# Optimization experiments

Hardware: AMD Instinct MI355X
Metric: run time of the kernel (lower is better)

Reference implementation:

```python
import jax, jax.numpy as jnp
import numpy as np

B, T, HS = 2, 2048, 4096
H, HK, D = 32, 8, 128  # num_heads, num_kv_heads, head_dim; HS == H*D
N_REP = H // HK


def setup_inputs() -> dict:
    key = jax.random.key(0)
    k1, k2, k3 = jax.random.split(key, 3)
    x = jax.random.normal(k1, (B, T, HS), dtype=jnp.float32)
    # qkv Linear (no bias): out_features = HS + 2*HK*D
    W_qkv = jax.random.normal(k2, (HS + 2 * HK * D, HS), dtype=jnp.float32) * 0.02
    W_proj = jax.random.normal(k3, (HS, HS), dtype=jnp.float32) * 0.02
    # Realistic RoPE cache (rotate-half convention): [1, T, 1, D]
    pos = jnp.arange(T, dtype=jnp.float32)
    inv_freq = 1.0 / (10000.0 ** (jnp.arange(0, D, 2, dtype=jnp.float32) / D))
    ang = pos[:, None] * inv_freq[None, :]                      # [T, D/2]
    rope_cos = jnp.concatenate([jnp.cos(ang), jnp.cos(ang)], -1)[None, :, None, :]
    rope_sin = jnp.concatenate([jnp.sin(ang), jnp.sin(ang)], -1)[None, :, None, :]
    return {"x": x, "rope_cos": rope_cos, "rope_sin": rope_sin,
            "W_qkv": W_qkv, "W_proj": W_proj}


def _rotate_half(u):
    u1, u2 = jnp.split(u, 2, axis=-1)
    return jnp.concatenate([-u2, u1], axis=-1)


def _apply_rope(u, cos, sin):
    return u * cos + _rotate_half(u) * sin


def reference(x, rope_cos, rope_sin, W_qkv, W_proj):
    # fused QKV projection
    qkv = jnp.einsum('btc,oc->bto', x, W_qkv)
    q, k, v = jnp.split(qkv, [HS, HS + HK * D], axis=-1)
    q = q.reshape(B, T, H, D)
    k = k.reshape(B, T, HK, D)
    v = v.reshape(B, T, HK, D)
    # inline RoPE on q and k
    q = _apply_rope(q, rope_cos[:, :T], rope_sin[:, :T])
    k = _apply_rope(k, rope_cos[:, :T], rope_sin[:, :T])
    # GQA repeat_kv: [B,T,HK,D] -> [B,T,H,D]
    k = jnp.repeat(k, N_REP, axis=2)
    v = jnp.repeat(v, N_REP, axis=2)
    # causal attention (flash-equivalent math)
    scale = 1.0 / jnp.sqrt(jnp.asarray(D, dtype=q.dtype))
    scores = jnp.einsum('bqhd,bkhd->bhqk', q, k) * scale        # [B,H,T,T]
    causal = jnp.tril(jnp.ones((T, T), dtype=bool))
    scores = jnp.where(causal[None, None], scores, jnp.finfo(scores.dtype).min)
    p = jax.nn.softmax(scores, axis=-1)
    out = jnp.einsum('bhqk,bkhd->bqhd', p, v).reshape(B, T, HS)
    return jnp.einsum('btc,oc->bto', out, W_proj)
```

## Files before the change

kernel.cpp:

```cpp
#include <hip/hip_runtime.h>
#include <hip/hip_bf16.h>

typedef __attribute__((ext_vector_type(8))) short short8;
typedef __attribute__((ext_vector_type(4))) short short4v;
typedef __attribute__((ext_vector_type(4))) float floatx4;

__device__ __forceinline__ float b2f(ushort u) {
  unsigned x = ((unsigned)u) << 16;
  return __builtin_bit_cast(float, x);
}
__device__ __forceinline__ ushort f2b(float f) {
  unsigned x = __builtin_bit_cast(unsigned, f);
  x += 0x7fffu + ((x >> 16) & 1u);
  return (ushort)(x >> 16);
}

__device__ __forceinline__ void gload_lds16(const void* g, void* l) {
  __builtin_amdgcn_global_load_lds(
      (const __attribute__((address_space(1))) unsigned int*)g,
      (__attribute__((address_space(3))) unsigned int*)l, 16, 0, 0);
}

__global__ __launch_bounds__(256) void cvt_kernel(const float* __restrict__ in,
                                                  ushort* __restrict__ out, long n) {
  long i0 = ((long)blockIdx.x * 256 + threadIdx.x) * 4;
  long stride = (long)gridDim.x * 256 * 4;
  for (long i = i0; i < n; i += stride) {
    float4 v = *(const float4*)(in + i);
    ushort4 u;
    u.x = f2b(v.x); u.y = f2b(v.y); u.z = f2b(v.z); u.w = f2b(v.w);
    *(ushort4*)(out + i) = u;
  }
}

template <int BN, int OUTBF16>
__global__ __launch_bounds__(512, 2)
void gemm_pipe(const ushort* __restrict__ A, const ushort* __restrict__ B,
               float* __restrict__ Cf, ushort* __restrict__ Cb,
               int M, int N, int K) {
  constexpr int BNF = BN / 64;
  __shared__ __align__(16) ushort sA[2][256 * 64];
  __shared__ __align__(16) ushort sB[2][BN * 64];
  const int t = threadIdx.x;
  const int lane = t & 63;
  const int L = lane & 15, g = lane >> 4;
  const int w = t >> 6;
  const int wr = w >> 2, wc = w & 3;
  const int ntn = N / BN;
  const int nwg = gridDim.x;
  const int wg = blockIdx.x;
  const int swz = (wg & 7) * (nwg >> 3) + (wg >> 3);
  const int m0 = (swz / ntn) << 8;
  const int n0 = (swz % ntn) * BN;

  floatx4 acc[8][BNF];
#pragma unroll
  for (int i = 0; i < 8; i++)
#pragma unroll
    for (int j = 0; j < BNF; j++) acc[i][j] = (floatx4)(0.0f);

  const ushort* Ab = A + (size_t)m0 * K;
  const ushort* Bb = B + (size_t)n0 * K;

  auto stage_tile = [&](const ushort* Ag, const ushort* Bg, int buf) {
#pragma unroll
    for (int j = 0; j < 4; j++) {
      const int c = j * 512 + t;
      const int row = c >> 3, ch = c & 7;
      const int kc = ch ^ (row & 7);
      gload_lds16(Ag + (size_t)row * K + kc * 8, (char*)&sA[buf][0] + c * 16);
    }
#pragma unroll
    for (int j = 0; j < BNF; j++) {
      const int c = j * 512 + t;
      const int row = c >> 3, ch = c & 7;
      const int kc = ch ^ (row & 7);
      gload_lds16(Bg + (size_t)row * K + kc * 8, (char*)&sB[buf][0] + c * 16);
    }
  };
  auto rdA = [&](int buf, int mh, int kc16, short8* dst) {
#pragma unroll
    for (int i = 0; i < 4; i++) {
      const int row = wr * 128 + mh * 64 + i * 16 + L;
      const int ch = (kc16 * 4 + g) ^ (row & 7);
      dst[i] = *(const short8*)((const char*)&sA[buf][0] + row * 128 + ch * 16);
    }
  };
  auto rdB = [&](int buf, int kc16, short8* dst) {
#pragma unroll
    for (int i = 0; i < BNF; i++) {
      const int row = wc * (BN / 4) + i * 16 + L;
      const int ch = (kc16 * 4 + g) ^ (row & 7);
      dst[i] = *(const short8*)((const char*)&sB[buf][0] + row * 128 + ch * 16);
    }
  };

  short8 a0[4], a1[4], b0[BNF], b1[BNF];

  auto mfmaN = [&](short8* af, short8* bf, int accbase, int cnt) {
    __builtin_amdgcn_s_setprio(1);
    for (int i = 0; i < cnt; i++)
#pragma unroll
      for (int nf = 0; nf < BNF; nf++)
        acc[accbase + i][nf] =
            __builtin_amdgcn_mfma_f32_16x16x32_bf16(af[i], bf[nf], acc[accbase + i][nf], 0, 0, 0);
    __builtin_amdgcn_s_setprio(0);
  };

  const int NT = K >> 6;
  stage_tile(Ab, Bb, 0);
  __syncthreads();
  rdA(0, 0, 0, a0);
  rdB(0, 0, b0);

  for (int T = 0; T < NT; ++T) {
    const int p = T & 1, q = p ^ 1;
    const bool more = (T + 1 < NT);
    if (more) stage_tile(Ab + (T + 1) * 64, Bb + (T + 1) * 64, q);
    rdA(p, 1, 0, a1);
    mfmaN(a0, b0, 0, 4);
    rdA(p, 0, 1, a0);
    rdB(p, 1, b1);
    mfmaN(a1, b0, 4, 4);
    rdA(p, 1, 1, a1);
    mfmaN(a0, b1, 0, 4);
    mfmaN(a1, b1, 4, 2);
    __syncthreads();
    if (more) {
      rdA(q, 0, 0, a0);
      rdB(q, 0, b0);
    }
    mfmaN(a1 + 2, b1, 6, 2);
  }

#pragma unroll
  for (int mf = 0; mf < 8; mf++)
#pragma unroll
    for (int nf = 0; nf < BNF; nf++)
#pragma unroll
      for (int r = 0; r < 4; r++) {
        const int row = m0 + wr * 128 + mf * 16 + g * 4 + r;
        const int col = n0 + wc * (BN / 4) + nf * 16 + L;
        if (OUTBF16)
          Cb[(size_t)row * N + col] = f2b(acc[mf][nf][r]);
        else
          Cf[(size_t)row * N + col] = acc[mf][nf][r];
      }
}

__global__ __launch_bounds__(256)
void rope_kernel(const ushort* __restrict__ qkv, const float* __restrict__ cosp,
                 const float* __restrict__ sinp, ushort* __restrict__ Qo,
                 ushort* __restrict__ Ko) {
  const int row = blockIdx.x;
  const int b = row >> 11, tt = row & 2047;
  const int i = threadIdx.x;
  const ushort* qr = qkv + (size_t)row * 6144;

  const int jb = (i & 7) * 8;
  float cs[8], sn[8];
  *(float4*)&cs[0] = *(const float4*)(cosp + tt * 128 + jb);
  *(float4*)&cs[4] = *(const float4*)(cosp + tt * 128 + jb + 4);
  *(float4*)&sn[0] = *(const float4*)(sinp + tt * 128 + jb);
  *(float4*)&sn[4] = *(const float4*)(sinp + tt * 128 + jb + 4);

  {
    const int hh = i >> 3;
    short8 lo = *(const short8*)(qr + hh * 128 + jb);
    short8 hi = *(const short8*)(qr + hh * 128 + 64 + jb);
    short8 olo, ohi;
#pragma unroll
    for (int e = 0; e < 8; e++) {
      float fl = b2f((ushort)lo[e]), fh = b2f((ushort)hi[e]);
      olo[e] = (short)f2b(fl * cs[e] - fh * sn[e]);
      ohi[e] = (short)f2b(fh * cs[e] + fl * sn[e]);
    }
    ushort* dst = Qo + ((size_t)(b * 32 + hh) * 2048 + tt) * 128 + jb;
    *(short8*)dst = olo;
    *(short8*)(dst + 64) = ohi;
  }
  if (i < 64) {
    const int hkk = i >> 3;
    short8 lo = *(const short8*)(qr + 4096 + hkk * 128 + jb);
    short8 hi = *(const short8*)(qr + 4096 + hkk * 128 + 64 + jb);
    short8 olo, ohi;
#pragma unroll
    for (int e = 0; e < 8; e++) {
      float fl = b2f((ushort)lo[e]), fh = b2f((ushort)hi[e]);
      olo[e] = (short)f2b(fl * cs[e] - fh * sn[e]);
      ohi[e] = (short)f2b(fh * cs[e] + fl * sn[e]);
    }
    ushort* dst = Ko + ((size_t)(b * 8 + hkk) * 2048 + tt) * 128 + jb;
    *(short8*)dst = olo;
    *(short8*)(dst + 64) = ohi;
  }
}

__global__ __launch_bounds__(256)
void vtrans_kernel(const ushort* __restrict__ qkv, ushort* __restrict__ Vt) {
  const int bx = blockIdx.x;
  const int t0 = (bx & 31) * 64;
  const int hk = (bx >> 5) & 7;
  const int b = bx >> 8;
  const int i = threadIdx.x;
  const int tq = i & 15;
  const int dn = i >> 4;
  const ushort* src = qkv + ((size_t)(b * 2048 + t0 + tq * 4)) * 6144 + 5120 + hk * 128 + dn * 8;
  short8 v0 = *(const short8*)(src);
  short8 v1 = *(const short8*)(src + 6144);
  short8 v2 = *(const short8*)(src + 12288);
  short8 v3 = *(const short8*)(src + 18432);
  ushort* dst = Vt + ((size_t)(b * 8 + hk) * 128 + dn * 8) * 2048 + t0 + tq * 4;
#pragma unroll
  for (int e = 0; e < 8; e++) {
    short4v pk;
    pk[0] = v0[e]; pk[1] = v1[e]; pk[2] = v2[e]; pk[3] = v3[e];
    *(short4v*)(dst + (size_t)e * 2048) = pk;
  }
}

#define ATT_SCALE 0.08838834764831845f

__global__ __launch_bounds__(256, 2)
void attn_kernel(const ushort* __restrict__ Q, const ushort* __restrict__ Kg,
                 const ushort* __restrict__ Vtg, ushort* __restrict__ O) {
  __shared__ __align__(16) ushort Klds[2][64 * 128];
  __shared__ __align__(16) ushort Vlds[2][128 * 64];
  __shared__ __align__(16) ushort Plds[4][32 * 64];
  const int t = threadIdx.x, lane = t & 63, w = t >> 6;
  const int bx = blockIdx.x;
  const int pair = bx & 7;
  const int h = (bx >> 3) & 31;
  const int b = bx >> 8;
  const int hk = h >> 2;
  const int qtA = pair, qtB = 15 - pair;
  const int nA = (qtA + 1) * 2, nB = (qtB + 1) * 2;
  const int total = nA + nB;

  const ushort* Qp = Q + ((size_t)(b * 32 + h) * 2048) * 128;
  const ushort* Kp = Kg + ((size_t)(b * 8 + hk) * 2048) * 128;
  const ushort* Vp = Vtg + ((size_t)(b * 8 + hk) * 128) * 2048;

  const int L = lane & 15, g = lane >> 4;

  auto stage = [&](int s) {
    const int tt = (s < nA) ? s : s - nA;
    const int kv0 = tt * 64;
    ushort* Kd = Klds[s & 1];
    ushort* Vd = Vlds[s & 1];
#pragma unroll
    for (int j = 0; j < 4; j++) {
      const int c = j * 256 + t;
      const int krow = c >> 4, kcol = c & 15;
      gload_lds16(Kp + (size_t)(kv0 + krow) * 128 + ((kcol ^ (krow & 15)) << 3),
                  (char*)Kd + c * 16);
    }
#pragma unroll
    for (int j = 0; j < 4; j++) {
      const int c = j * 256 + t;
      const int d = c >> 3, tc = c & 7;
      gload_lds16(Vp + (size_t)d * 2048 + kv0 + ((tc ^ (d & 7)) << 3),
                  (char*)Vd + c * 16);
    }
  };

  short8 qf[2][4];
  floatx4 o[2][8];
  float mrun[2][4], lrun[2][4];

  auto init_pass = [&](int qw) {
#pragma unroll
    for (int m = 0; m < 2; m++) {
#pragma unroll
      for (int kc = 0; kc < 4; kc++)
        qf[m][kc] = *(const short8*)(Qp + (size_t)(qw + m * 16 + L) * 128 + kc * 32 + g * 8);
#pragma unroll
      for (int dt = 0; dt < 8; dt++) o[m][dt] = (floatx4)(0.0f);
#pragma unroll
      for (int r = 0; r < 4; r++) { mrun[m][r] = -3.0e38f; lrun[m][r] = 0.0f; }
    }
  };

  auto compute = [&](int tt, int bsel, int qw) {
    const int kv0 = tt * 64;
    if (kv0 > qw + 31) return;
    const ushort* Kd = Klds[bsel];
    const ushort* Vd = Vlds[bsel];
    ushort* Pw = Plds[w];
    floatx4 sfr[2][4];
#pragma unroll
    for (int m = 0; m < 2; m++)
#pragma unroll
      for (int n = 0; n < 4; n++) sfr[m][n] = (floatx4)(0.0f);
#pragma unroll
    for (int kc = 0; kc < 4; kc++) {
#pragma unroll
      for (int n = 0; n < 4; n++) {
        const int krow = n * 16 + L;
        const int ck = ((kc << 2) + g) ^ L;
        short8 kf = *(const short8*)((const char*)Kd + krow * 256 + ck * 16);
        sfr[0][n] = __builtin_amdgcn_mfma_f32_16x16x32_bf16(qf[0][kc], kf, sfr[0][n], 0, 0, 0);
        sfr[1][n] = __builtin_amdgcn_mfma_f32_16x16x32_bf16(qf[1][kc], kf, sfr[1][n], 0, 0, 0);
      }
    }
    float mx[2][4];
#pragma unroll
    for (int m = 0; m < 2; m++)
#pragma unroll
      for (int r = 0; r < 4; r++) {
        const int qg = qw + m * 16 + g * 4 + r;
        float mm = -3.0e38f;
#pragma unroll
        for (int n = 0; n < 4; n++) {
          float v = sfr[m][n][r] * ATT_SCALE;
          if (kv0 + n * 16 + L > qg) v = -1e30f;
          sfr[m][n][r] = v;
          mm = fmaxf(mm, v);
        }
        mx[m][r] = mm;
      }
#pragma unroll
    for (int off = 1; off < 16; off <<= 1)
#pragma unroll
      for (int m = 0; m < 2; m++)
#pragma unroll
        for (int r = 0; r < 4; r++)
          mx[m][r] = fmaxf(mx[m][r], __shfl_xor(mx[m][r], off, 64));
    float alpha[2][4], ls[2][4];
#pragma unroll
    for (int m = 0; m < 2; m++)
#pragma unroll
      for (int r = 0; r < 4; r++) {
        float mnew = fmaxf(mrun[m][r], mx[m][r]);
        alpha[m][r] = __expf(mrun[m][r] - mnew);
        mrun[m][r] = mnew;
        ls[m][r] = 0.0f;
      }
#pragma unroll
    for (int m = 0; m < 2; m++)
#pragma unroll
      for (int n = 0; n < 4; n++)
#pragma unroll
        for (int r = 0; r < 4; r++) {
          float p = __expf(sfr[m][n][r] - mrun[m][r]);
          sfr[m][n][r] = p;
          ls[m][r] += p;
        }
#pragma unroll
    for (int off = 1; off < 16; off <<= 1)
#pragma unroll
      for (int m = 0; m < 2; m++)
#pragma unroll
        for (int r = 0; r < 4; r++)
          ls[m][r] += __shfl_xor(ls[m][r], off, 64);
#pragma unroll
    for (int m = 0; m < 2; m++)
#pragma unroll
      for (int r = 0; r < 4; r++)
        lrun[m][r] = lrun[m][r] * alpha[m][r] + ls[m][r];
#pragma unroll
    for (int m = 0; m < 2; m++)
#pragma unroll
      for (int n = 0; n < 4; n++)
#pragma unroll
        for (int r = 0; r < 4; r++) {
          const int R = m * 16 + g * 4 + r;
          const int col = n * 16 + L;
          Pw[R * 64 + (col ^ (r << 4))] = f2b(sfr[m][n][r]);
        }
#pragma unroll
    for (int m = 0; m < 2; m++)
#pragma unroll
      for (int dt = 0; dt < 8; dt++)
#pragma unroll
        for (int r = 0; r < 4; r++) o[m][dt][r] *= alpha[m][r];
#pragma unroll
    for (int kc = 0; kc < 2; kc++) {
      short8 pf[2];
#pragma unroll
      for (int m = 0; m < 2; m++) {
        const int R = m * 16 + L;
        const int C = kc * 32 + g * 8;
        pf[m] = *(const short8*)&Pw[R * 64 + (C ^ ((L & 3) << 4))];
      }
#pragma unroll
      for (int dt = 0; dt < 8; dt++) {
        const int d = dt * 16 + L;
        const int gp = ((kc << 2) + g) ^ (d & 7);
        short8 vf = *(const short8*)((const char*)Vd + d * 128 + gp * 16);
        o[0][dt] = __builtin_amdgcn_mfma_f32_16x16x32_bf16(pf[0], vf, o[0][dt], 0, 0, 0);
        o[1][dt] = __builtin_amdgcn_mfma_f32_16x16x32_bf16(pf[1], vf, o[1][dt], 0, 0, 0);
      }
    }
  };

  auto epilogue = [&](int qw) {
#pragma unroll
    for (int m = 0; m < 2; m++)
#pragma unroll
      for (int r = 0; r < 4; r++) {
        const float inv = 1.0f / lrun[m][r];
        const int qg = qw + m * 16 + g * 4 + r;
#pragma unroll
        for (int dt = 0; dt < 8; dt++)
          O[(size_t)(b * 2048 + qg) * 4096 + h * 128 + dt * 16 + L] =
              f2b(o[m][dt][r] * inv);
      }
  };

  int s = 0;
  stage(0);
  __syncthreads();

  int qw = qtA * 128 + w * 32;
  init_pass(qw);
  for (int i = 0; i < nA; ++i, ++s) {
    if (s + 1 < total) stage(s + 1);
    compute(i, s & 1, qw);
    __syncthreads();
  }
  epilogue(qw);

  qw = qtB * 128 + w * 32;
  init_pass(qw);
  for (int i = 0; i < nB; ++i, ++s) {
    if (s + 1 < total) stage(s + 1);
    compute(i, s & 1, qw);
    __syncthreads();
  }
  epilogue(qw);
}

extern "C" void kernel_launch(void* const* d_in, const int* in_sizes, int n_in,
                              void* d_out, int out_size, void* d_ws, size_t ws_size,
                              hipStream_t stream) {
  const float* x = (const float*)d_in[0];
  const float* rc = (const float*)d_in[1];
  const float* rs = (const float*)d_in[2];
  const float* wqkv = (const float*)d_in[3];
  const float* wproj = (const float*)d_in[4];
  float* out = (float*)d_out;

  ushort* xb = (ushort*)d_ws;
  ushort* wqkvb = xb + 16777216;
  ushort* qkvb = wqkvb + 25165824;
  ushort* Qb = qkvb + 25165824;
  ushort* Kb = Qb + 16777216;
  ushort* Vt = Kb + 4194304;
  ushort* wprojb = xb;
  ushort* aob = qkvb;

  cvt_kernel<<<2048, 256, 0, stream>>>(x, xb, 16777216L);
  cvt_kernel<<<2048, 256, 0, stream>>>(wqkv, wqkvb, 25165824L);
  gemm_pipe<192, 1><<<512, 512, 0, stream>>>(xb, wqkvb, nullptr, qkvb, 4096, 6144, 4096);
  rope_kernel<<<4096, 256, 0, stream>>>(qkvb, rc, rs, Qb, Kb);
  vtrans_kernel<<<512, 256, 0, stream>>>(qkvb, Vt);
  attn_kernel<<<512, 256, 0, stream>>>(Qb, Kb, Vt, aob);
  cvt_kernel<<<2048, 256, 0, stream>>>(wproj, wprojb, 16777216L);
  gemm_pipe<256, 0><<<256, 512, 0, stream>>>(aob, wprojb, out, nullptr, 4096, 4096, 4096);
}
```

Measured before the change: 541.3 us.

## Triple-buffer GEMM LDS staging with prefetch two tiles ahead and BN=128

The bf16 GEMM moves from double to triple LDS buffering, so global-to-LDS loads for tile T+2 are issued while tile T is computed. The full __syncthreads is replaced by an explicit vmcnt/lgkmcnt wait plus a raw s_barrier, so only the older stage has to land before each barrier. Both GEMM launches switch to BN=128 with more workgroups, which makes the hard-coded vmcnt(6) count match the six loads per stage. The aim is to hide global memory latency better; the cost is more LDS per block and lower per-block arithmetic intensity from the narrower N tile.

```diff
diff --git a/kernel.cpp b/kernel.cpp
--- a/kernel.cpp
+++ b/kernel.cpp
@@ -39,8 +39,8 @@
                float* __restrict__ Cf, ushort* __restrict__ Cb,
                int M, int N, int K) {
   constexpr int BNF = BN / 64;
-  __shared__ __align__(16) ushort sA[2][256 * 64];
-  __shared__ __align__(16) ushort sB[2][BN * 64];
+  __shared__ __align__(16) ushort sA[3][256 * 64];
+  __shared__ __align__(16) ushort sB[3][BN * 64];
   const int t = threadIdx.x;
   const int lane = t & 63;
   const int L = lane & 15, g = lane >> 4;
@@ -71,7 +71,7 @@
       gload_lds16(Ag + (size_t)row * K + kc * 8, (char*)&sA[buf][0] + c * 16);
     }
 #pragma unroll
-    for (int j = 0; j < BNF; j++) {
+    for (int j = 0; j < BN / 64; j++) {
       const int c = j * 512 + t;
       const int row = c >> 3, ch = c & 7;
       const int kc = ch ^ (row & 7);
@@ -109,28 +109,39 @@
 
   const int NT = K >> 6;
   stage_tile(Ab, Bb, 0);
-  __syncthreads();
+  stage_tile(Ab + 64, Bb + 64, 1);
+  asm volatile("s_waitcnt vmcnt(6)" ::: "memory");
+  __builtin_amdgcn_s_barrier();
+  __builtin_amdgcn_sched_barrier(0);
   rdA(0, 0, 0, a0);
   rdB(0, 0, b0);
 
+  int bp = 0;
   for (int T = 0; T < NT; ++T) {
-    const int p = T & 1, q = p ^ 1;
-    const bool more = (T + 1 < NT);
-    if (more) stage_tile(Ab + (T + 1) * 64, Bb + (T + 1) * 64, q);
-    rdA(p, 1, 0, a1);
+    const int bq = (bp == 2) ? 0 : bp + 1;
+    const int bs = (bq == 2) ? 0 : bq + 1;
+    if (T + 2 < NT)
+      stage_tile(Ab + (size_t)(T + 2) * 64, Bb + (size_t)(T + 2) * 64, bs);
+    rdA(bp, 1, 0, a1);
     mfmaN(a0, b0, 0, 4);
-    rdA(p, 0, 1, a0);
-    rdB(p, 1, b1);
+    rdA(bp, 0, 1, a0);
+    rdB(bp, 1, b1);
     mfmaN(a1, b0, 4, 4);
-    rdA(p, 1, 1, a1);
+    rdA(bp, 1, 1, a1);
     mfmaN(a0, b1, 0, 4);
     mfmaN(a1, b1, 4, 2);
-    __syncthreads();
-    if (more) {
-      rdA(q, 0, 0, a0);
-      rdB(q, 0, b0);
+    if (T + 1 < NT) {
+      if (T + 2 < NT)
+        asm volatile("s_waitcnt vmcnt(6) lgkmcnt(0)" ::: "memory");
+      else
+        asm volatile("s_waitcnt vmcnt(0) lgkmcnt(0)" ::: "memory");
+      __builtin_amdgcn_s_barrier();
+      __builtin_amdgcn_sched_barrier(0);
+      rdA(bq, 0, 0, a0);
+      rdB(bq, 0, b0);
     }
     mfmaN(a1 + 2, b1, 6, 2);
+    bp = bq;
   }
 
 #pragma unroll
@@ -452,10 +463,10 @@
 
   cvt_kernel<<<2048, 256, 0, stream>>>(x, xb, 16777216L);
   cvt_kernel<<<2048, 256, 0, stream>>>(wqkv, wqkvb, 25165824L);
-  gemm_pipe<192, 1><<<512, 512, 0, stream>>>(xb, wqkvb, nullptr, qkvb, 4096, 6144, 4096);
+  gemm_pipe<128, 1><<<768, 512, 0, stream>>>(xb, wqkvb, nullptr, qkvb, 4096, 6144, 4096);
   rope_kernel<<<4096, 256, 0, stream>>>(qkvb, rc, rs, Qb, Kb);
   vtrans_kernel<<<512, 256, 0, stream>>>(qkvb, Vt);
   attn_kernel<<<512, 256, 0, stream>>>(Qb, Kb, Vt, aob);
   cvt_kernel<<<2048, 256, 0, stream>>>(wproj, wprojb, 16777216L);
-  gemm_pipe<256, 0><<<256, 512, 0, stream>>>(aob, wprojb, out, nullptr, 4096, 4096, 4096);
-}
+  gemm_pipe<128, 0><<<512, 512, 0, stream>>>(aob, wprojb, out, nullptr, 4096, 4096, 4096);
+}
```

Measured after the change: 662.8 us. 22.4% more time.
